# Performance work log

Hardware: AMD Instinct MI355X
Metric: run time of the kernel (lower is better)

The kernel has to match this reference:

```python
import jax, jax.numpy as jnp
import numpy as np

B, D, E, H = 8192, 512, 16, 128  # batch, input_dim, num_experts, hidden_dim
EPS = 1e-5  # BatchNorm eps (torch default)


def setup_inputs() -> dict:
    key = jax.random.key(0)
    ks = iter(jax.random.split(key, 32))
    def n(shape, s=0.05):
        return jax.random.normal(next(ks), shape, dtype=jnp.float32) * s
    inp = {"x": jax.random.normal(next(ks), (B, D), dtype=jnp.float32)}
    # Router params, stacked over the 2 branches (gender, race)
    inp["rbn_gamma"] = jnp.ones((2, D), jnp.float32)
    inp["rbn_beta"] = jnp.zeros((2, D), jnp.float32)
    inp["rbn_mean"] = n((2, D))
    inp["rbn_var"] = jnp.ones((2, D), jnp.float32)
    inp["rW1"], inp["rb1"] = n((2, D, 64)), jnp.full((2, 64), 0.1, jnp.float32)
    inp["rW2"], inp["rb2"] = n((2, 64, 32)), jnp.full((2, 32), 0.1, jnp.float32)
    inp["rW3"], inp["rb3"] = n((2, 32, E)), jnp.full((2, E), 0.1, jnp.float32)
    # Expert params, stacked over [branch=2, expert=16]
    inp["ebn_gamma"] = jnp.ones((2, E, D), jnp.float32)
    inp["ebn_beta"] = jnp.zeros((2, E, D), jnp.float32)
    inp["ebn_mean"] = n((2, E, D))
    inp["ebn_var"] = jnp.ones((2, E, D), jnp.float32)
    inp["eW1"], inp["eb1"] = n((2, E, D, H)), jnp.full((2, E, H), 0.1, jnp.float32)
    inp["eW2"], inp["eb2"] = n((2, E, H, H // 2)), jnp.full((2, E, H // 2), 0.1, jnp.float32)
    inp["eW3"], inp["eb3"] = n((2, E, H // 2)), jnp.full((2, E), 0.1, jnp.float32)
    inp["branch_weights"] = jnp.array([0.5, 0.5], jnp.float32)
    return inp


def reference(x, rbn_gamma, rbn_beta, rbn_mean, rbn_var, rW1, rb1, rW2, rb2,
              rW3, rb3, ebn_gamma, ebn_beta, ebn_mean, ebn_var, eW1, eb1,
              eW2, eb2, eW3, eb3, branch_weights):
    def branch(c):
        # Router: BN(eval) -> Linear(64) -> ReLU -> Linear(32) -> ReLU -> Linear(E) -> Softmax
        xn = (x - rbn_mean[c]) * jax.lax.rsqrt(rbn_var[c] + EPS) * rbn_gamma[c] + rbn_beta[c]
        h = jax.nn.relu(xn @ rW1[c] + rb1[c])
        h = jax.nn.relu(h @ rW2[c] + rb2[c])
        rw = jax.nn.softmax(h @ rW3[c] + rb3[c], axis=1)  # [B, E]
        # Experts batched over E: per-expert BN(eval) -> Linear -> ReLU -> Linear -> ReLU -> Linear -> sigmoid
        m, v = ebn_mean[c][:, None, :], ebn_var[c][:, None, :]
        g, b = ebn_gamma[c][:, None, :], ebn_beta[c][:, None, :]
        xe = (x[None] - m) * jax.lax.rsqrt(v + EPS) * g + b          # [E, B, D]
        h1 = jax.nn.relu(jnp.einsum('ebd,edh->ebh', xe, eW1[c]) + eb1[c][:, None, :])
        h2 = jax.nn.relu(jnp.einsum('ebh,ehk->ebk', h1, eW2[c]) + eb2[c][:, None, :])
        out = jax.nn.sigmoid(jnp.einsum('ebk,ek->eb', h2, eW3[c]) + eb3[c][:, None])  # [E, B]
        return jnp.einsum('be,eb->b', rw, out)                        # weighted sum over experts
    gender_pred = branch(0)
    race_pred = branch(1)
    return branch_weights[0] * gender_pred + branch_weights[1] * race_pred
```

## Files before the change

### kernel.cpp

```cpp
#include <hip/hip_runtime.h>

typedef __attribute__((ext_vector_type(8))) short short8;
typedef __attribute__((ext_vector_type(8))) unsigned short ushort8;
typedef __attribute__((ext_vector_type(4))) float f32x4;
typedef unsigned int u32;
typedef unsigned short u16;

#define AS_GLOBAL(p) ((const __attribute__((address_space(1))) u32*)(p))
#define AS_LDS(p) ((__attribute__((address_space(3))) u32*)(p))

#define NB 8192
#define ND 512
#define NH 128

#define OFF_XPK    0u
#define OFF_W1PK   8388608u
#define OFF_W2PK   12582912u
#define OFF_RW1PT  13107200u
#define OFF_B1P    13238272u
#define OFF_RB1P   13254656u
#define OFF_RWT    13255168u
#define OFF_PBIAS  14303744u

__device__ __forceinline__ u16 f2bf(float f) {
  union { float f; u32 u; } v; v.f = f;
  return (u16)((v.u + 0x7FFFu + ((v.u >> 16) & 1u)) >> 16);
}

__global__ __launch_bounds__(256) void k_prep_all(
    const float* __restrict__ x, u16* __restrict__ xpk,
    const float* __restrict__ eg, const float* __restrict__ ebb,
    const float* __restrict__ em, const float* __restrict__ ev,
    const float* __restrict__ eW1, u16* __restrict__ w1pk, float* __restrict__ pbias,
    const float* __restrict__ eW2, u16* __restrict__ w2pk,
    const float* __restrict__ rbn_g, const float* __restrict__ rbn_b,
    const float* __restrict__ rbn_m, const float* __restrict__ rbn_v,
    const float* __restrict__ rW1, const float* __restrict__ rb1,
    u16* __restrict__ rw1pt, float* __restrict__ rb1p,
    float* __restrict__ out)
{
  __shared__ __align__(16) unsigned char sh[17920];
  const int blk = blockIdx.x, t = threadIdx.x;
  if (blk < 2048) {
    int i = (blk * 256 + t) * 8;
    const float4* p = (const float4*)(x + i);
    float4 v0 = p[0], v1 = p[1];
    ushort8 r;
    r[0] = f2bf(v0.x); r[1] = f2bf(v0.y); r[2] = f2bf(v0.z); r[3] = f2bf(v0.w);
    r[4] = f2bf(v1.x); r[5] = f2bf(v1.y); r[6] = f2bf(v1.z); r[7] = f2bf(v1.w);
    int row = i >> 9, k0 = i & 511;
    int rb = row >> 4, lr = row & 15, kb = k0 >> 5, q = (k0 >> 3) & 3;
    *(ushort8*)(xpk + ((u32)(rb * 16 + kb) * 64 + q * 16 + lr) * 8) = r;
  } else if (blk < 2304) {
    float* sa = (float*)sh;
    float* sc = sa + 64;
    u16* tile = (u16*)(sc + 64);
    float* pb2 = (float*)(tile + 64 * 128);
    const int pair = (blk - 2048) >> 3, dc = (blk - 2048) & 7;
    const int d0 = dc * 64;
    if (t < 64) {
      int d = pair * ND + d0 + t;
      float a = eg[d] * rsqrtf(ev[d] + 1e-5f);
      sa[t] = a;
      sc[t] = ebb[d] - em[d] * a;
    }
    __syncthreads();
    const int h = t & 127, pr = t >> 7;
    float acc = 0.f;
    const float* src = eW1 + (size_t)pair * ND * NH + (size_t)d0 * NH;
#pragma unroll
    for (int i = 0; i < 32; ++i) {
      int dl = i * 2 + pr;
      float w = src[dl * NH + h];
      tile[dl * 128 + h] = f2bf(w * sa[dl]);
      acc += w * sc[dl];
    }
    pb2[pr * 128 + h] = acc;
    __syncthreads();
    {
      int hh = t >> 1, half = t & 1;
      const int nb = hh >> 4, lr = hh & 15;
#pragma unroll
      for (int v8 = 0; v8 < 4; ++v8) {
        int db = d0 + half * 32 + v8 * 8;
        int kb = db >> 5, q = (db >> 3) & 3;
        ushort8 r;
#pragma unroll
        for (int j = 0; j < 8; ++j) r[j] = tile[(half * 32 + v8 * 8 + j) * 128 + hh];
        *(ushort8*)(w1pk + (u32)((pair * 16 + kb) * 8 + nb) * 512 + (q * 16 + lr) * 8) = r;
      }
    }
    if (t < 128) pbias[(u32)(pair * 8 + dc) * 128 + t] = pb2[t] + pb2[128 + t];
  } else if (blk < 2336) {
    const int pair = blk - 2304;
    const float* w2 = eW2 + (size_t)pair * NH * 64;
    int n = t & 63, kk = t >> 6;
    for (int k = kk * 32; k < kk * 32 + 32; ++k) {
      u32 dst = ((u32)((pair * 4 + (k >> 5)) * 4 + (n >> 4))) * 512
              + (((k >> 3) & 3) * 16 + (n & 15)) * 8 + (k & 7);
      w2pk[dst] = f2bf(w2[k * 64 + n]);
    }
  } else if (blk < 2338) {
    const int c = blk - 2336;
    int n = t >> 2, q = t & 3;
    const float* g  = rbn_g + c * ND;
    const float* b  = rbn_b + c * ND;
    const float* m  = rbn_m + c * ND;
    const float* vv = rbn_v + c * ND;
    const float* w1 = rW1 + (size_t)c * ND * 64;
    float acc = 0.f;
    for (int d = q * 128; d < q * 128 + 128; ++d) {
      float a  = g[d] * rsqrtf(vv[d] + 1e-5f);
      float cc = b[d] - m[d] * a;
      float w  = w1[d * 64 + n];
      rw1pt[((u32)c * 64 + n) * ND + d] = f2bf(a * w);
      acc += cc * w;
    }
    acc += __shfl_xor(acc, 1, 64);
    acc += __shfl_xor(acc, 2, 64);
    if (q == 0) rb1p[c * 64 + n] = rb1[c * 64 + n] + acc;
  } else {
    float4 z; z.x = 0.f; z.y = 0.f; z.z = 0.f; z.w = 0.f;
    float4* o4 = (float4*)out;
#pragma unroll
    for (int j = 0; j < 8; ++j) o4[t * 8 + j] = z;
  }
}

__global__ __launch_bounds__(256) void k_router(
    const u16* __restrict__ xpk, const u16* __restrict__ rw1pt,
    const float* __restrict__ rb1p, const float* __restrict__ rW2,
    const float* __restrict__ rb2, const float* __restrict__ rW3,
    const float* __restrict__ rb3, float* __restrict__ rwT,
    const float* __restrict__ pbias, const float* __restrict__ eb1,
    float* __restrict__ b1p)
{
  __shared__ float h1l[64][65];
  __shared__ float h2l[64][33];
  __shared__ float w2s[2048];
  __shared__ float w3s[512];
  const int tid = threadIdx.x;
  if (blockIdx.x >= 256) {
    const int pair = blockIdx.x - 256;
    if (tid < 128) {
      float s = eb1[pair * NH + tid];
#pragma unroll
      for (int dc = 0; dc < 8; ++dc) s += pbias[(u32)(pair * 8 + dc) * 128 + tid];
      b1p[pair * NH + tid] = s;
    }
    return;
  }
  const int lane = tid & 63;
  const int wv = tid >> 6;
  const int q = lane >> 4;
  const int lr = lane & 15;
  const int c = blockIdx.x >> 7;
  const int r0 = (blockIdx.x & 127) * 64;

  {
    const float* W2 = rW2 + c * 2048;
    *(float4*)(w2s + tid * 8)     = *(const float4*)(W2 + tid * 8);
    *(float4*)(w2s + tid * 8 + 4) = *(const float4*)(W2 + tid * 8 + 4);
    if (tid < 128)
      *(float4*)(w3s + tid * 4) = *(const float4*)(rW3 + c * 512 + tid * 4);
  }

  f32x4 acc[4] = {};
  const u16* xfr   = xpk + ((u32)((r0 >> 4) + wv) * 16) * 512 + (u32)lane * 8;
  const u16* wbase = rw1pt + ((u32)c * 64 << 9);
  for (int kb = 0; kb < 16; ++kb) {
    short8 a = *(const short8*)(xfr + kb * 512);
#pragma unroll
    for (int u = 0; u < 4; ++u) {
      short8 b = *(const short8*)(wbase + (((u32)(u * 16 + lr)) << 9) + kb * 32 + q * 8);
      acc[u] = __builtin_amdgcn_mfma_f32_16x16x32_bf16(a, b, acc[u], 0, 0, 0);
    }
  }
#pragma unroll
  for (int u = 0; u < 4; ++u) {
    int n = u * 16 + lr;
    float bias = rb1p[c * 64 + n];
#pragma unroll
    for (int i = 0; i < 4; ++i) {
      float v = acc[u][i] + bias;
      h1l[wv * 16 + q * 4 + i][n] = v > 0.f ? v : 0.f;
    }
  }
  __syncthreads();
  {
    int row = tid >> 2, part = (tid & 3) * 8;
    float hv[8];
#pragma unroll
    for (int j = 0; j < 8; ++j) hv[j] = rb2[c * 32 + part + j];
#pragma unroll
    for (int k = 0; k < 64; ++k) {
      float hk = h1l[row][k];
#pragma unroll
      for (int j = 0; j < 8; ++j) hv[j] += hk * w2s[k * 32 + part + j];
    }
#pragma unroll
    for (int j = 0; j < 8; ++j) h2l[row][part + j] = hv[j] > 0.f ? hv[j] : 0.f;
  }
  __syncthreads();
  {
    int row = tid >> 2, e0 = (tid & 3) * 4;
    float lg[4];
#pragma unroll
    for (int e = 0; e < 4; ++e) {
      float a3 = rb3[c * 16 + e0 + e];
#pragma unroll
      for (int k = 0; k < 32; ++k) a3 += h2l[row][k] * w3s[k * 16 + e0 + e];
      lg[e] = a3;
    }
    float mx = fmaxf(fmaxf(lg[0], lg[1]), fmaxf(lg[2], lg[3]));
    mx = fmaxf(mx, __shfl_xor(mx, 1, 64));
    mx = fmaxf(mx, __shfl_xor(mx, 2, 64));
    float sm = 0.f;
#pragma unroll
    for (int e = 0; e < 4; ++e) { lg[e] = __expf(lg[e] - mx); sm += lg[e]; }
    sm += __shfl_xor(sm, 1, 64);
    sm += __shfl_xor(sm, 2, 64);
    float inv = 1.f / sm;
#pragma unroll
    for (int e = 0; e < 4; ++e)
      rwT[(u32)(c * 16 + e0 + e) * NB + r0 + row] = lg[e] * inv;
  }
}

__global__ __launch_bounds__(512, 2) void k_expert(
    const u16* __restrict__ xpk, const u16* __restrict__ w1pk,
    const float* __restrict__ b1p, const u16* __restrict__ w2pk,
    const float* __restrict__ eb2, const float* __restrict__ eW3,
    const float* __restrict__ eb3, const float* __restrict__ rwT,
    const float* __restrict__ bw, float* __restrict__ out)
{
  __shared__ __align__(16) unsigned char smem[65536];
  const int tid = threadIdx.x;
  const int lane = tid & 63;
  const int wv = tid >> 6;
  const int q = lane >> 4, lr = lane & 15;
  const int p = wv >> 2;
  const int wq = wv & 3;
  const int xcd  = blockIdx.x & 7;
  const int slot = blockIdx.x >> 3;
  const int pt   = xcd * 2 + (slot >> 5);
  const int bt   = slot & 31;
  const int pr0  = pt * 2;
  const int r0   = bt * 256;

  const u32 lane16 = (u32)lane * 16;

  const u16* stbase;
  u32 stlds, ststep, stjmul;
  if (wv < 4) {
    stbase = xpk + ((u32)(bt * 16 + wv * 4) * 16) * 512 + (u32)lane * 8;
    stlds  = (u32)wv * 4096;
    ststep = 512;
    stjmul = 8192;
  } else {
    const int g0 = (wv - 4) * 4;
    stbase = w1pk + ((u32)(pr0 + (g0 >> 3)) * 128 + (g0 & 7)) * 512 + (u32)lane * 8;
    stlds  = 16384 + (u32)(wv - 4) * 4096;
    ststep = 4096;
    stjmul = 512;
  }

#define STAGE(BUF, KB) do { \
  _Pragma("unroll") for (int j_ = 0; j_ < 4; ++j_) \
    __builtin_amdgcn_global_load_lds( \
        AS_GLOBAL(stbase + j_ * stjmul + (u32)(KB) * ststep), \
        AS_LDS(smem + (BUF) + stlds + j_ * 1024), 16, 0, 0); \
  } while (0)

  f32x4 acc[4][8] = {};

  STAGE(0, 0);
  STAGE(32768, 1);
  asm volatile("s_waitcnt vmcnt(4)" ::: "memory");
  __builtin_amdgcn_s_barrier();
  __builtin_amdgcn_sched_barrier(0);

#pragma unroll
  for (int kb = 0; kb < 16; ++kb) {
    const u32 BUF = (u32)(kb & 1) * 32768;
    short8 a_[4], b_[8];
#pragma unroll
    for (int t = 0; t < 4; ++t)
      a_[t] = *(const short8*)(smem + BUF + (u32)(wq * 4 + t) * 1024 + lane16);
#pragma unroll
    for (int u = 0; u < 8; ++u)
      b_[u] = *(const short8*)(smem + BUF + 16384 + (u32)(p * 8 + u) * 1024 + lane16);
    asm volatile("s_waitcnt lgkmcnt(0)" ::: "memory");
    __builtin_amdgcn_sched_barrier(0);
    if (kb < 14) {
      __builtin_amdgcn_s_barrier();
      __builtin_amdgcn_sched_barrier(0);
      STAGE(BUF, kb + 2);
      __builtin_amdgcn_sched_barrier(0);
    }
    __builtin_amdgcn_s_setprio(1);
#pragma unroll
    for (int t = 0; t < 4; ++t)
#pragma unroll
      for (int u = 0; u < 8; ++u)
        acc[t][u] = __builtin_amdgcn_mfma_f32_16x16x32_bf16(a_[t], b_[u], acc[t][u], 0, 0, 0);
    __builtin_amdgcn_s_setprio(0);
    __builtin_amdgcn_sched_barrier(0);
    if (kb < 14)       asm volatile("s_waitcnt vmcnt(4)" ::: "memory");
    else if (kb == 14) asm volatile("s_waitcnt vmcnt(0)" ::: "memory");
    if (kb < 15) {
      __builtin_amdgcn_s_barrier();
      __builtin_amdgcn_sched_barrier(0);
    }
  }
#undef STAGE

  __syncthreads();

#pragma unroll
  for (int pass = 0; pass < 2; ++pass) {
    const int pairG = pr0 + pass;
    if (p == pass) {
      float b1w[8];
#pragma unroll
      for (int u = 0; u < 8; ++u) b1w[u] = b1p[pairG * NH + u * 16 + lr];
#pragma unroll
      for (int t = 0; t < 4; ++t)
#pragma unroll
        for (int u = 0; u < 8; ++u) {
          const int rb = wq * 4 + t, kbh = u >> 1;
          const int qq = (u & 1) * 2 + (lr >> 3), jj = lr & 7;
#pragma unroll
          for (int i = 0; i < 4; ++i) {
            float v = acc[t][u][i] + b1w[u];
            v = v > 0.f ? v : 0.f;
            u32 byteoff = ((u32)((rb * 4 + kbh) * 64 + qq * 16 + q * 4 + i)) * 16 + jj * 2;
            *(u16*)(smem + byteoff) = f2bf(v);
          }
        }
    }
    __syncthreads();

    f32x4 acc2[2][4] = {};
#pragma unroll
    for (int kk = 0; kk < 4; ++kk) {
      short8 a2[2], b2[4];
#pragma unroll
      for (int t2 = 0; t2 < 2; ++t2)
        a2[t2] = *(const short8*)(smem + ((u32)((wv * 2 + t2) * 4 + kk)) * 1024 + lane16);
#pragma unroll
      for (int u2 = 0; u2 < 4; ++u2)
        b2[u2] = *(const short8*)(w2pk + ((u32)((pairG * 4 + kk) * 4 + u2)) * 512 + (u32)lane * 8);
#pragma unroll
      for (int t2 = 0; t2 < 2; ++t2)
#pragma unroll
        for (int u2 = 0; u2 < 4; ++u2)
          acc2[t2][u2] = __builtin_amdgcn_mfma_f32_16x16x32_bf16(a2[t2], b2[u2], acc2[t2][u2], 0, 0, 0);
    }

    {
      float bb2[4], bw3v[4];
#pragma unroll
      for (int u2 = 0; u2 < 4; ++u2) {
        bb2[u2]  = eb2[pairG * 64 + u2 * 16 + lr];
        bw3v[u2] = eW3[pairG * 64 + u2 * 16 + lr];
      }
      float b3 = eb3[pairG];
      float bwc = bw[pairG >> 4];
#pragma unroll
      for (int t2 = 0; t2 < 2; ++t2) {
        float pp[4] = {0.f, 0.f, 0.f, 0.f};
#pragma unroll
        for (int u2 = 0; u2 < 4; ++u2)
#pragma unroll
          for (int i = 0; i < 4; ++i) {
            float h = acc2[t2][u2][i] + bb2[u2];
            h = h > 0.f ? h : 0.f;
            pp[i] += h * bw3v[u2];
          }
#pragma unroll
        for (int m = 1; m < 16; m <<= 1)
#pragma unroll
          for (int i = 0; i < 4; ++i) pp[i] += __shfl_xor(pp[i], m, 64);
        if (lr == 0) {
#pragma unroll
          for (int i = 0; i < 4; ++i) {
            int row = wv * 32 + t2 * 16 + q * 4 + i;
            float z = pp[i] + b3;
            float s = 1.f / (1.f + __expf(-z));
            float rw = rwT[(u32)pairG * NB + r0 + row];
            atomicAdd(out + r0 + row, bwc * rw * s);
          }
        }
      }
    }
    __syncthreads();
  }
}

extern "C" void kernel_launch(void* const* d_in, const int* in_sizes, int n_in,
                              void* d_out, int out_size, void* d_ws, size_t ws_size,
                              hipStream_t stream) {
  const float* x     = (const float*)d_in[0];
  const float* rbn_g = (const float*)d_in[1];
  const float* rbn_b = (const float*)d_in[2];
  const float* rbn_m = (const float*)d_in[3];
  const float* rbn_v = (const float*)d_in[4];
  const float* rW1   = (const float*)d_in[5];
  const float* rb1   = (const float*)d_in[6];
  const float* rW2   = (const float*)d_in[7];
  const float* rb2   = (const float*)d_in[8];
  const float* rW3   = (const float*)d_in[9];
  const float* rb3   = (const float*)d_in[10];
  const float* ebn_g = (const float*)d_in[11];
  const float* ebn_b = (const float*)d_in[12];
  const float* ebn_m = (const float*)d_in[13];
  const float* ebn_v = (const float*)d_in[14];
  const float* eW1   = (const float*)d_in[15];
  const float* eb1   = (const float*)d_in[16];
  const float* eW2   = (const float*)d_in[17];
  const float* eb2   = (const float*)d_in[18];
  const float* eW3   = (const float*)d_in[19];
  const float* eb3   = (const float*)d_in[20];
  const float* bw    = (const float*)d_in[21];

  char* ws = (char*)d_ws;
  u16*   xpk   = (u16*)(ws + OFF_XPK);
  u16*   w1pk  = (u16*)(ws + OFF_W1PK);
  u16*   w2pk  = (u16*)(ws + OFF_W2PK);
  u16*   rw1pt = (u16*)(ws + OFF_RW1PT);
  float* b1p   = (float*)(ws + OFF_B1P);
  float* rb1p  = (float*)(ws + OFF_RB1P);
  float* rwT   = (float*)(ws + OFF_RWT);
  float* pbias = (float*)(ws + OFF_PBIAS);
  float* outf  = (float*)d_out;

  k_prep_all<<<dim3(2339), dim3(256), 0, stream>>>(
      x, xpk, ebn_g, ebn_b, ebn_m, ebn_v, eW1, w1pk, pbias, eW2, w2pk,
      rbn_g, rbn_b, rbn_m, rbn_v, rW1, rb1, rw1pt, rb1p, outf);
  k_router<<<dim3(288), dim3(256), 0, stream>>>(
      xpk, rw1pt, rb1p, rW2, rb2, rW3, rb3, rwT, pbias, eb1, b1p);
  k_expert<<<dim3(512), dim3(512), 0, stream>>>(
      xpk, w1pk, b1p, w2pk, eb2, eW3, eb3, rwT, bw, outf);
}
```

Baseline: 92.18 us.

## Shrink expert tiles, simplify staging pipeline, replace atomics with combine kernel

Expert blocks shrink from 512 threads × 256 rows to 256 threads × 128 rows, giving 1024 blocks, and the LDS double buffer shrinks to 48KB. The staging now prefetches only one k-step ahead, with full vmcnt(0) waits and no setprio. The atomicAdd into out, which needed the output zeroed first, is replaced by writing bf16 sigmoid outputs to a scratch buffer and running a separate k_combine kernel that does the router-weighted sum. This removes atomic contention and the zeroing pass, at the cost of an extra launch, extra traffic, and bf16 rounding of the expert outputs.

```diff
diff --git a/kernel.cpp b/kernel.cpp
--- a/kernel.cpp
+++ b/kernel.cpp
@@ -17,14 +17,19 @@
 #define OFF_W1PK   8388608u
 #define OFF_W2PK   12582912u
 #define OFF_RW1PT  13107200u
-#define OFF_B1P    13238272u
-#define OFF_RB1P   13254656u
-#define OFF_RWT    13255168u
-#define OFF_PBIAS  14303744u
+#define OFF_RB1P   13238272u
+#define OFF_PBIAS  13238784u
+#define OFF_B1P    13369856u
+#define OFF_RWT    13402112u
+#define OFF_ST     14450688u
 
 __device__ __forceinline__ u16 f2bf(float f) {
   union { float f; u32 u; } v; v.f = f;
   return (u16)((v.u + 0x7FFFu + ((v.u >> 16) & 1u)) >> 16);
+}
+__device__ __forceinline__ float bf2f(u16 h) {
+  union { u32 u; float f; } v; v.u = (u32)h << 16;
+  return v.f;
 }
 
 __global__ __launch_bounds__(256) void k_prep_all(
@@ -36,8 +41,7 @@
     const float* __restrict__ rbn_g, const float* __restrict__ rbn_b,
     const float* __restrict__ rbn_m, const float* __restrict__ rbn_v,
     const float* __restrict__ rW1, const float* __restrict__ rb1,
-    u16* __restrict__ rw1pt, float* __restrict__ rb1p,
-    float* __restrict__ out)
+    u16* __restrict__ rw1pt, float* __restrict__ rb1p)
 {
   __shared__ __align__(16) unsigned char sh[17920];
   const int blk = blockIdx.x, t = threadIdx.x;
@@ -100,7 +104,7 @@
               + (((k >> 3) & 3) * 16 + (n & 15)) * 8 + (k & 7);
       w2pk[dst] = f2bf(w2[k * 64 + n]);
     }
-  } else if (blk < 2338) {
+  } else {
     const int c = blk - 2336;
     int n = t >> 2, q = t & 3;
     const float* g  = rbn_g + c * ND;
@@ -119,11 +123,6 @@
     acc += __shfl_xor(acc, 1, 64);
     acc += __shfl_xor(acc, 2, 64);
     if (q == 0) rb1p[c * 64 + n] = rb1[c * 64 + n] + acc;
-  } else {
-    float4 z; z.x = 0.f; z.y = 0.f; z.z = 0.f; z.w = 0.f;
-    float4* o4 = (float4*)out;
-#pragma unroll
-    for (int j = 0; j < 8; ++j) o4[t * 8 + j] = z;
   }
 }
 
@@ -156,7 +155,6 @@
   const int lr = lane & 15;
   const int c = blockIdx.x >> 7;
   const int r0 = (blockIdx.x & 127) * 64;
-
   {
     const float* W2 = rW2 + c * 2048;
     *(float4*)(w2s + tid * 8)     = *(const float4*)(W2 + tid * 8);
@@ -164,7 +162,6 @@
     if (tid < 128)
       *(float4*)(w3s + tid * 4) = *(const float4*)(rW3 + c * 512 + tid * 4);
   }
-
   f32x4 acc[4] = {};
   const u16* xfr   = xpk + ((u32)((r0 >> 4) + wv) * 16) * 512 + (u32)lane * 8;
   const u16* wbase = rw1pt + ((u32)c * 64 << 9);
@@ -227,95 +224,79 @@
   }
 }
 
-__global__ __launch_bounds__(512, 2) void k_expert(
-    const u16* __restrict__ xpk, const u16* __restrict__ w1pk,
-    const float* __restrict__ b1p, const u16* __restrict__ w2pk,
+__global__ __launch_bounds__(256, 2) void k_expert(
+    const u16* __restrict__ xpk, const float* __restrict__ b1p,
+    const u16* __restrict__ w2pk,
     const float* __restrict__ eb2, const float* __restrict__ eW3,
-    const float* __restrict__ eb3, const float* __restrict__ rwT,
-    const float* __restrict__ bw, float* __restrict__ out)
+    const float* __restrict__ eb3, u16* __restrict__ sT)
 {
-  __shared__ __align__(16) unsigned char smem[65536];
+  __shared__ __align__(16) unsigned char smem[49152];
   const int tid = threadIdx.x;
   const int lane = tid & 63;
   const int wv = tid >> 6;
   const int q = lane >> 4, lr = lane & 15;
-  const int p = wv >> 2;
-  const int wq = wv & 3;
+  const int wr = wv >> 1;
+  const int p  = wv & 1;
   const int xcd  = blockIdx.x & 7;
   const int slot = blockIdx.x >> 3;
-  const int pt   = xcd * 2 + (slot >> 5);
-  const int bt   = slot & 31;
+  const int pt   = xcd * 2 + (slot >> 6);
+  const int bt   = slot & 63;
   const int pr0  = pt * 2;
-  const int r0   = bt * 256;
-
+  const int r0   = bt * 128;
   const u32 lane16 = (u32)lane * 16;
 
-  const u16* stbase;
-  u32 stlds, ststep, stjmul;
-  if (wv < 4) {
-    stbase = xpk + ((u32)(bt * 16 + wv * 4) * 16) * 512 + (u32)lane * 8;
-    stlds  = (u32)wv * 4096;
-    ststep = 512;
-    stjmul = 8192;
-  } else {
-    const int g0 = (wv - 4) * 4;
-    stbase = w1pk + ((u32)(pr0 + (g0 >> 3)) * 128 + (g0 & 7)) * 512 + (u32)lane * 8;
-    stlds  = 16384 + (u32)(wv - 4) * 4096;
-    ststep = 4096;
-    stjmul = 512;
+  u32 soff[6], sstep[6], slds[6];
+#pragma unroll
+  for (int j = 0; j < 6; ++j) {
+    int f = wv * 6 + j;
+    if (f < 8) {
+      soff[j]  = ((u32)(bt * 8 + f) * 16) * 512 + (u32)lane * 8;
+      sstep[j] = 512;
+      slds[j]  = (u32)f * 1024;
+    } else {
+      int g = f - 8;
+      soff[j]  = 4194304u + ((u32)(pr0 + (g >> 3)) * 128 + (g & 7)) * 512 + (u32)lane * 8;
+      sstep[j] = 4096;
+      slds[j]  = 8192 + (u32)g * 1024;
+    }
   }
 
 #define STAGE(BUF, KB) do { \
-  _Pragma("unroll") for (int j_ = 0; j_ < 4; ++j_) \
+  _Pragma("unroll") for (int j_ = 0; j_ < 6; ++j_) \
     __builtin_amdgcn_global_load_lds( \
-        AS_GLOBAL(stbase + j_ * stjmul + (u32)(KB) * ststep), \
-        AS_LDS(smem + (BUF) + stlds + j_ * 1024), 16, 0, 0); \
+        AS_GLOBAL(xpk + soff[j_] + (u32)(KB) * sstep[j_]), \
+        AS_LDS(smem + (BUF) + slds[j_]), 16, 0, 0); \
   } while (0)
 
   f32x4 acc[4][8] = {};
 
   STAGE(0, 0);
-  STAGE(32768, 1);
-  asm volatile("s_waitcnt vmcnt(4)" ::: "memory");
+  asm volatile("s_waitcnt vmcnt(0)" ::: "memory");
   __builtin_amdgcn_s_barrier();
-  __builtin_amdgcn_sched_barrier(0);
 
 #pragma unroll
   for (int kb = 0; kb < 16; ++kb) {
-    const u32 BUF = (u32)(kb & 1) * 32768;
+    const u32 BUF = (u32)(kb & 1) * 24576;
+    if (kb < 15) {
+      STAGE(BUF ^ 24576, kb + 1);
+      __builtin_amdgcn_sched_barrier(0);
+    }
     short8 a_[4], b_[8];
 #pragma unroll
     for (int t = 0; t < 4; ++t)
-      a_[t] = *(const short8*)(smem + BUF + (u32)(wq * 4 + t) * 1024 + lane16);
+      a_[t] = *(const short8*)(smem + BUF + (u32)(wr * 4 + t) * 1024 + lane16);
 #pragma unroll
     for (int u = 0; u < 8; ++u)
-      b_[u] = *(const short8*)(smem + BUF + 16384 + (u32)(p * 8 + u) * 1024 + lane16);
-    asm volatile("s_waitcnt lgkmcnt(0)" ::: "memory");
-    __builtin_amdgcn_sched_barrier(0);
-    if (kb < 14) {
-      __builtin_amdgcn_s_barrier();
-      __builtin_amdgcn_sched_barrier(0);
-      STAGE(BUF, kb + 2);
-      __builtin_amdgcn_sched_barrier(0);
-    }
-    __builtin_amdgcn_s_setprio(1);
+      b_[u] = *(const short8*)(smem + BUF + 8192 + (u32)(p * 8 + u) * 1024 + lane16);
 #pragma unroll
     for (int t = 0; t < 4; ++t)
 #pragma unroll
       for (int u = 0; u < 8; ++u)
         acc[t][u] = __builtin_amdgcn_mfma_f32_16x16x32_bf16(a_[t], b_[u], acc[t][u], 0, 0, 0);
-    __builtin_amdgcn_s_setprio(0);
-    __builtin_amdgcn_sched_barrier(0);
-    if (kb < 14)       asm volatile("s_waitcnt vmcnt(4)" ::: "memory");
-    else if (kb == 14) asm volatile("s_waitcnt vmcnt(0)" ::: "memory");
-    if (kb < 15) {
-      __builtin_amdgcn_s_barrier();
-      __builtin_amdgcn_sched_barrier(0);
-    }
+    if (kb < 15) asm volatile("s_waitcnt vmcnt(0)" ::: "memory");
+    __builtin_amdgcn_s_barrier();
   }
 #undef STAGE
-
-  __syncthreads();
 
 #pragma unroll
   for (int pass = 0; pass < 2; ++pass) {
@@ -328,13 +309,14 @@
       for (int t = 0; t < 4; ++t)
 #pragma unroll
         for (int u = 0; u < 8; ++u) {
-          const int rb = wq * 4 + t, kbh = u >> 1;
-          const int qq = (u & 1) * 2 + (lr >> 3), jj = lr & 7;
+          const int rb = wr * 4 + t;
+          const int kb2 = u >> 1;
+          const int q2 = (u & 1) * 2 + (lr >> 3), j2 = lr & 7;
 #pragma unroll
           for (int i = 0; i < 4; ++i) {
             float v = acc[t][u][i] + b1w[u];
             v = v > 0.f ? v : 0.f;
-            u32 byteoff = ((u32)((rb * 4 + kbh) * 64 + qq * 16 + q * 4 + i)) * 16 + jj * 2;
+            u32 byteoff = ((u32)((rb * 4 + kb2) * 64 + q2 * 16 + q * 4 + i)) * 16 + j2 * 2;
             *(u16*)(smem + byteoff) = f2bf(v);
           }
         }
@@ -347,7 +329,7 @@
       short8 a2[2], b2[4];
 #pragma unroll
       for (int t2 = 0; t2 < 2; ++t2)
-        a2[t2] = *(const short8*)(smem + ((u32)((wv * 2 + t2) * 4 + kk)) * 1024 + lane16);
+        a2[t2] = *(const short8*)(smem + (u32)((wv * 2 + t2) * 4 + kk) * 1024 + lane16);
 #pragma unroll
       for (int u2 = 0; u2 < 4; ++u2)
         b2[u2] = *(const short8*)(w2pk + ((u32)((pairG * 4 + kk) * 4 + u2)) * 512 + (u32)lane * 8);
@@ -366,7 +348,6 @@
         bw3v[u2] = eW3[pairG * 64 + u2 * 16 + lr];
       }
       float b3 = eb3[pairG];
-      float bwc = bw[pairG >> 4];
 #pragma unroll
       for (int t2 = 0; t2 < 2; ++t2) {
         float pp[4] = {0.f, 0.f, 0.f, 0.f};
@@ -388,14 +369,28 @@
             int row = wv * 32 + t2 * 16 + q * 4 + i;
             float z = pp[i] + b3;
             float s = 1.f / (1.f + __expf(-z));
-            float rw = rwT[(u32)pairG * NB + r0 + row];
-            atomicAdd(out + r0 + row, bwc * rw * s);
+            sT[(u32)pairG * NB + r0 + row] = f2bf(s);
           }
         }
       }
     }
     __syncthreads();
   }
+}
+
+__global__ __launch_bounds__(256) void k_combine(
+    const float* __restrict__ rwT, const u16* __restrict__ sT,
+    const float* __restrict__ bw, float* __restrict__ out)
+{
+  int b = blockIdx.x * 256 + threadIdx.x;
+  float bw0 = bw[0], bw1 = bw[1];
+  float acc0 = 0.f, acc1 = 0.f;
+#pragma unroll
+  for (int e = 0; e < 16; ++e) {
+    acc0 += rwT[(u32)e * NB + b] * bf2f(sT[(u32)e * NB + b]);
+    acc1 += rwT[(u32)(16 + e) * NB + b] * bf2f(sT[(u32)(16 + e) * NB + b]);
+  }
+  out[b] = bw0 * acc0 + bw1 * acc1;
 }
 
 extern "C" void kernel_launch(void* const* d_in, const int* in_sizes, int n_in,
@@ -429,17 +424,19 @@
   u16*   w1pk  = (u16*)(ws + OFF_W1PK);
   u16*   w2pk  = (u16*)(ws + OFF_W2PK);
   u16*   rw1pt = (u16*)(ws + OFF_RW1PT);
+  float* rb1p  = (float*)(ws + OFF_RB1P);
+  float* pbias = (float*)(ws + OFF_PBIAS);
   float* b1p   = (float*)(ws + OFF_B1P);
-  float* rb1p  = (float*)(ws + OFF_RB1P);
   float* rwT   = (float*)(ws + OFF_RWT);
-  float* pbias = (float*)(ws + OFF_PBIAS);
+  u16*   sT    = (u16*)(ws + OFF_ST);
   float* outf  = (float*)d_out;
 
-  k_prep_all<<<dim3(2339), dim3(256), 0, stream>>>(
+  k_prep_all<<<dim3(2338), dim3(256), 0, stream>>>(
       x, xpk, ebn_g, ebn_b, ebn_m, ebn_v, eW1, w1pk, pbias, eW2, w2pk,
-      rbn_g, rbn_b, rbn_m, rbn_v, rW1, rb1, rw1pt, rb1p, outf);
+      rbn_g, rbn_b, rbn_m, rbn_v, rW1, rb1, rw1pt, rb1p);
   k_router<<<dim3(288), dim3(256), 0, stream>>>(
       xpk, rw1pt, rb1p, rW2, rb2, rW3, rb3, rwT, pbias, eb1, b1p);
-  k_expert<<<dim3(512), dim3(512), 0, stream>>>(
-      xpk, w1pk, b1p, w2pk, eb2, eW3, eb3, rwT, bw, outf);
-}
+  k_expert<<<dim3(1024), dim3(256), 0, stream>>>(
+      xpk, b1p, w2pk, eb2, eW3, eb3, sT);
+  k_combine<<<dim3(NB / 256), dim3(256), 0, stream>>>(rwT, sT, bw, outf);
+}
```

After: 95.86 us. 1.04x slower.
